# Optimization experiments

Hardware: AMD Instinct MI355X
Metric: run time of the kernel (lower is better)

Reference implementation:

```python
import jax, jax.numpy as jnp
import numpy as np

B, T, N, D = 32, 336, 321, 3
G = 512          # global_hidden
L = 2            # layer_nums
E = 4            # experts per layer
K = 2            # top-k
F = 2048         # d_ff (expert hidden)
P = 96           # pred_len
LOSS_COEF = 0.01


def setup_inputs() -> dict:
    key = jax.random.key(0)
    ks = iter(jax.random.split(key, 24))
    rn = lambda shape, s=0.02: jax.random.normal(next(ks), shape, jnp.float32) * s
    return {
        "x": jax.random.normal(next(ks), (B, T, N, D), jnp.float32),
        # GlobalEmbedding
        "Wv": rn((N, 1)), "bv": jnp.zeros((1,), jnp.float32),
        "Wt": rn((T, G)), "bt": jnp.zeros((G,), jnp.float32),
        # CrossAttention
        "Wq": rn((G, G)), "bq": jnp.zeros((G,), jnp.float32),
        "Wk": rn((G, G)), "bk": jnp.zeros((G,), jnp.float32),
        "Wva": rn((G, G)), "bva": jnp.zeros((G,), jnp.float32),
        # AMS MoE layers (stacked over L)
        "Wg": rn((L, T, E)),
        "We1": rn((L, E, T, F)), "be1": jnp.zeros((L, E, F), jnp.float32),
        "We2": rn((L, E, F, T)), "be2": jnp.zeros((L, E, T), jnp.float32),
        # projections head
        "P1w": rn((T, P)), "P1b": jnp.zeros((P,), jnp.float32),
        "P2w": rn((P, 2 * P)), "P2b": jnp.zeros((2 * P,), jnp.float32),
    }


def _cv_squared(v):
    return v.var() / (v.mean() ** 2 + 1e-10)


def reference(x, Wv, bv, Wt, bt, Wq, bq, Wk, bk, Wva, bva,
              Wg, We1, be1, We2, be2, P1w, P1b, P2w, P2b):
    Bv, Tv, Nv, Dv = x.shape
    # ---- GlobalEmbedding: (B,T,N,D) -> (B,D,G), with the original's raw reshape
    g = jnp.einsum('btvd,vo->btdo', x, Wv)[..., 0] + bv[0]        # (B,T,D)
    g2 = g.reshape(Bv * Dv, Tv) @ Wt + bt                          # faithful contiguous reshape
    gf = g2.reshape(Bv, Dv, -1)                                    # (B,D,G)
    # ---- CrossAttention (no sqrt(d) scaling, per source)
    q = gf @ Wq + bq
    kk = gf @ Wk + bk
    v = gf @ Wva + bva
    attn = jax.nn.softmax(jnp.einsum('big,bjg->bij', q, kk), axis=-1)
    sst_attended = jnp.einsum('bij,bjg->big', attn, v)[:, 0, :]    # unused: use_attend=0
    del sst_attended
    # ---- slice value channel + RevIN norm over time
    x0 = x[..., 0]                                                 # (B,T,N)
    mu = x0.mean(axis=1, keepdims=True)
    sd = jnp.sqrt(x0.var(axis=1, keepdims=True) + 1e-5)
    out = (x0 - mu) / sd
    # ---- AMS layers: clean top-k gated MoE over per-node seq MLP experts
    balance_loss = jnp.float32(0.0)
    for l in range(L):
        logits = out.mean(axis=2) @ Wg[l]                          # (B,E)
        topv, topi = jax.lax.top_k(logits, K)
        gates = jnp.zeros_like(logits).at[
            jnp.arange(Bv)[:, None], topi].set(jax.nn.softmax(topv, axis=-1))
        importance = gates.sum(axis=0)
        balance_loss = balance_loss + _cv_squared(importance) * LOSS_COEF
        xt = out.transpose(0, 2, 1)                                # (B,N,T)
        h = jax.nn.relu(jnp.einsum('bnt,etf->ebnf', xt, We1[l])
                        + be1[l][:, None, None, :])                # (E,B,N,F)
        eo = jnp.einsum('ebnf,eft->ebnt', h, We2[l]) + be2[l][:, None, None, :]
        moe = jnp.einsum('be,ebnt->bnt', gates, eo).transpose(0, 2, 1)
        out = out + moe                                            # residual_connection=1
    # ---- projection head
    o = out.transpose(0, 2, 1)                                     # (B,N,T)
    hproj = jnp.tanh(o @ P1w + P1b)
    p = (hproj @ P2w + P2b).reshape(Bv, Nv, P, 2).transpose(0, 2, 1, 3)  # (B,P,N,2)
    mean = p[..., 0]
    std = jax.nn.softplus(p[..., 1]) + 1e-6
    return mean, balance_loss, std
```

## Files before the change

kernel.cpp:

```cpp
#include <hip/hip_runtime.h>
#include <hip/hip_bf16.h>
#include <cstdint>
#include <math.h>

#define B_ 32
#define T_ 336
#define N_ 321
#define L_ 2
#define E_ 4
#define F_ 2048
#define P_ 96
#define TPAD 352
#define NPAD 384

typedef __hip_bfloat16 bf16;
typedef __attribute__((ext_vector_type(8))) __bf16 bf16x8;
typedef __attribute__((ext_vector_type(4))) float f32x4;


__device__ __forceinline__ void async_copy16(const void* g, void* l) {
  __builtin_amdgcn_global_load_lds(
      (__attribute__((address_space(1))) void*)(uintptr_t)g,
      (__attribute__((address_space(3))) void*)(unsigned int)(uintptr_t)l,
      16, 0, 0);
}

__device__ __forceinline__ void pipe_barrier_vm0() {
  asm volatile("s_waitcnt vmcnt(0)" ::: "memory");
  __builtin_amdgcn_s_barrier();
  __builtin_amdgcn_sched_barrier(0);
}

__device__ __forceinline__ void pipe_barrier_full() {
  asm volatile("s_waitcnt vmcnt(0) lgkmcnt(0)" ::: "memory");
  __builtin_amdgcn_s_barrier();
  __builtin_amdgcn_sched_barrier(0);
}

__global__ void transpose_cast_kernel(const float* __restrict__ src, bf16* __restrict__ dst,
                                      int R, int C, int Rp, int Cp,
                                      long long sStride, long long dStride) {
  __shared__ float tile[32][33];
  const float* s = src + (size_t)blockIdx.z * sStride;
  bf16* d = dst + (size_t)blockIdx.z * dStride;
  int r0 = blockIdx.x * 32, c0 = blockIdx.y * 32;
  int tx = threadIdx.x, ty = threadIdx.y;
  #pragma unroll
  for (int ii = 0; ii < 4; ii++) {
    int rl = ty * 4 + ii;
    int r = r0 + rl, c = c0 + tx;
    tile[rl][tx] = (r < R && c < C) ? s[(size_t)r * C + c] : 0.f;
  }
  __syncthreads();
  #pragma unroll
  for (int ii = 0; ii < 4; ii++) {
    int cl = ty * 4 + ii;
    int cd = c0 + cl, rd = r0 + tx;
    if (cd < Cp && rd < Rp)
      d[(size_t)cd * Rp + rd] = __float2bfloat16(tile[tx][cl]);
  }
}

__global__ void repack_w2_kernel(const float* __restrict__ src, bf16* __restrict__ dst) {
  __shared__ float tile[32][96];
  int le = blockIdx.z, tb = blockIdx.y, f0 = blockIdx.x * 32;
  int tid = threadIdx.x;
  const float* s = src + (size_t)le * F_ * T_;
  for (int idx = tid; idx < 32 * 96; idx += 256) {
    int ff = idx / 96, tt = idx % 96;
    int t = tb * 96 + tt;
    tile[ff][tt] = (t < T_) ? s[(size_t)(f0 + ff) * T_ + t] : 0.f;
  }
  __syncthreads();
  bf16* d = dst + ((size_t)le * 4 + tb) * 196608 + (size_t)(f0 >> 3) * 768;
  for (int s2 = tid; s2 < 384; s2 += 256) {
    int kgl = s2 / 96, row = s2 % 96;
    bf16 v[8];
    #pragma unroll
    for (int j = 0; j < 8; j++) v[j] = __float2bfloat16(tile[kgl * 8 + j][row]);
    *(uint4*)(d + (size_t)kgl * 768 + row * 8) = *(const uint4*)v;
  }
}

__global__ __launch_bounds__(512) void revin_kernel(const float* __restrict__ x,
                                                    float* __restrict__ out,
                                                    bf16* __restrict__ Abuf) {
  __shared__ float red[8][64][2];
  __shared__ float minv[64][2];
  __shared__ unsigned int Lt[64][177];

  const int b = blockIdx.x;
  const int n0 = blockIdx.y * 64;
  const int tid = threadIdx.x;
  const int nl = tid & 63, tq = tid >> 6;
  const int n = n0 + nl;
  const bool valid = (n < N_);
  const float* xp = x + ((size_t)b * T_ * N_ + n) * 3;
  const int tbeg = tq * 42, tend = tbeg + 42;

  float s1 = 0.f, s2 = 0.f;
  if (valid) {
    for (int t = tbeg; t < tend; t++) {
      float v = xp[(size_t)t * N_ * 3];
      s1 += v; s2 += v * v;
    }
  }
  red[tq][nl][0] = s1; red[tq][nl][1] = s2;
  __syncthreads();
  if (tid < 64) {
    float a = 0.f, c = 0.f;
    #pragma unroll
    for (int q = 0; q < 8; q++) { a += red[q][tid][0]; c += red[q][tid][1]; }
    float mu = a / (float)T_;
    float var = c / (float)T_ - mu * mu;
    minv[tid][0] = mu;
    minv[tid][1] = 1.f / sqrtf(var + 1e-5f);
  }
  {
    int r = tid >> 3, c = 168 + (tid & 7);
    Lt[r][c] = 0u;
  }
  __syncthreads();

  const float mu = minv[nl][0], inv = minv[nl][1];
  for (int t = tbeg; t < tend; t += 2) {
    float v0 = 0.f, v1 = 0.f;
    if (valid) {
      v0 = (xp[(size_t)t * N_ * 3] - mu) * inv;
      v1 = (xp[(size_t)(t + 1) * N_ * 3] - mu) * inv;
      out[((size_t)b * T_ + t) * N_ + n] = v0;
      out[((size_t)b * T_ + t + 1) * N_ + n] = v1;
    }
    bf16 h0 = __float2bfloat16(v0), h1 = __float2bfloat16(v1);
    unsigned int u = (unsigned int)*(unsigned short*)&h0 |
                     ((unsigned int)*(unsigned short*)&h1 << 16);
    Lt[nl][t >> 1] = u;
  }
  __syncthreads();

  unsigned int* abase = (unsigned int*)(Abuf + ((size_t)b * NPAD + n0) * TPAD);
  #pragma unroll
  for (int k = 0; k < 22; k++) {
    int idx = tid + k * 512;
    int row = idx / 176, c = idx % 176;
    abase[(size_t)row * (TPAD / 2) + c] = Lt[row][c];
  }
}

__global__ void gate1_kernel(const float* __restrict__ out, float* __restrict__ colsum) {
  int b = blockIdx.y;
  int w = threadIdx.x >> 6, lane = threadIdx.x & 63;
  int t = blockIdx.x * 16 + w * 4;
  #pragma unroll
  for (int i = 0; i < 4; i++, t++) {
    const float* p = out + ((size_t)b * T_ + t) * N_;
    float s = 0.f;
    for (int n = lane; n < N_; n += 64) s += p[n];
    #pragma unroll
    for (int off = 32; off; off >>= 1) s += __shfl_down(s, off);
    if (lane == 0) colsum[b * T_ + t] = s;
  }
}

__global__ void gate2_kernel(const float* __restrict__ colsum, const float* __restrict__ Wg,
                             int* __restrict__ pair_e, float* __restrict__ pair_gate,
                             float* __restrict__ loss_partial, int layer) {
  __shared__ float lg[32][4];
  __shared__ float gates[32][4];
  __shared__ float imp[4];
  int tid = threadIdx.x;
  if (tid < 128) {
    int b = tid >> 2, e = tid & 3;
    float s = 0.f;
    for (int t = 0; t < T_; t++)
      s += colsum[b * T_ + t] * Wg[(layer * T_ + t) * E_ + e];
    lg[b][e] = s / (float)N_;
  }
  __syncthreads();
  if (tid < 32) {
    float v[4];
    #pragma unroll
    for (int e = 0; e < 4; e++) v[e] = lg[tid][e];
    int i0 = 0;
    for (int e = 1; e < 4; e++) if (v[e] > v[i0]) i0 = e;
    int i1 = -1;
    for (int e = 0; e < 4; e++) {
      if (e == i0) continue;
      if (i1 < 0 || v[e] > v[i1]) i1 = e;
    }
    float ex = expf(v[i1] - v[i0]);
    float g0 = 1.f / (1.f + ex);
    float g1 = ex / (1.f + ex);
    pair_e[tid * 2] = i0; pair_e[tid * 2 + 1] = i1;
    pair_gate[tid * 2] = g0; pair_gate[tid * 2 + 1] = g1;
    #pragma unroll
    for (int e = 0; e < 4; e++) gates[tid][e] = 0.f;
    gates[tid][i0] = g0; gates[tid][i1] = g1;
  }
  __syncthreads();
  if (tid < 4) {
    float s = 0.f;
    for (int bb = 0; bb < 32; bb++) s += gates[bb][tid];
    imp[tid] = s;
  }
  __syncthreads();
  if (tid == 0) {
    float m = (imp[0] + imp[1] + imp[2] + imp[3]) * 0.25f;
    float va = 0.f;
    #pragma unroll
    for (int e = 0; e < 4; e++) { float d = imp[e] - m; va += d * d; }
    va *= 0.25f;
    loss_partial[layer] = 0.01f * (va / (m * m + 1e-10f));
  }
}

__global__ __launch_bounds__(256) void gemm1_kernel(
    const bf16* __restrict__ Abuf, const bf16* __restrict__ W1T,
    const float* __restrict__ be1, const int* __restrict__ pair_e,
    const float* __restrict__ pair_gate, bf16* __restrict__ h, int layer) {
  __shared__ __align__(16) bf16 S1[16384];
  __shared__ float bias_s[128];

  const int tid = threadIdx.x;
  const int w = tid >> 6, lane = tid & 63;
  const int pair = blockIdx.z;
  const int b = pair >> 1;
  const int e = pair_e[pair];
  const float gate = pair_gate[pair];
  const int m0 = blockIdx.y * 128;
  const int f0 = blockIdx.x * 128;

  const bf16* Ag = Abuf + (size_t)b * NPAD * TPAD + (size_t)m0 * TPAD;
  const bf16* Bg = W1T + ((size_t)(layer * E_ + e) * F_ + f0) * TPAD;
  if (tid < 128) bias_s[tid] = be1[(size_t)(layer * E_ + e) * F_ + f0 + tid];

  f32x4 acc[4][4];
  const f32x4 zero = {0.f, 0.f, 0.f, 0.f};
  #pragma unroll
  for (int i = 0; i < 4; i++)
    #pragma unroll
    for (int j = 0; j < 4; j++) acc[i][j] = zero;

  const int wm = w >> 1, wn = w & 1;
  const int lrow = lane >> 2;
  const int lkoff = (lane & 3) * 8;
  const int quad = lane >> 4;
  const int l15 = lane & 15;

  auto stage1 = [&](int k, int buf) {
    const int k0 = k * 32;
    bf16* As = S1 + buf * 8192;
    bf16* Bs = As + 4096;
    #pragma unroll
    for (int i = 0; i < 2; i++) {
      int r = (w * 2 + i) * 16 + lrow;
      async_copy16(Ag + (size_t)r * TPAD + k0 + lkoff, As + (w * 2 + i) * 512);
      async_copy16(Bg + (size_t)r * TPAD + k0 + lkoff, Bs + (w * 2 + i) * 512);
    }
  };

  stage1(0, 0);
  pipe_barrier_full();

  for (int kk = 0; kk < TPAD / 32; ++kk) {
    if (kk < TPAD / 32 - 1) stage1(kk + 1, (kk + 1) & 1);
    const bf16* As = S1 + (kk & 1) * 8192;
    const bf16* Bs = As + 4096;
    bf16x8 af[4], bfr[4];
    #pragma unroll
    for (int mi = 0; mi < 4; mi++)
      af[mi] = *(const bf16x8*)(As + (wm * 64 + mi * 16 + l15) * 32 + quad * 8);
    #pragma unroll
    for (int ni = 0; ni < 4; ni++)
      bfr[ni] = *(const bf16x8*)(Bs + (wn * 64 + ni * 16 + l15) * 32 + quad * 8);
    #pragma unroll
    for (int mi = 0; mi < 4; mi++)
      #pragma unroll
      for (int ni = 0; ni < 4; ni++)
        acc[mi][ni] = __builtin_amdgcn_mfma_f32_16x16x32_bf16(af[mi], bfr[ni], acc[mi][ni], 0, 0, 0);
    pipe_barrier_vm0();
  }

  bf16* tw0 = S1 + w * 1024;
  bf16* tw1 = S1 + 4096 + w * 1024;
  size_t hb = (size_t)pair * 786432 + (size_t)((m0 >> 6) + wm) * 131072;
  const int kgbase = (f0 >> 3) + wn * 8 + (lane & 3) * 2;
  #pragma unroll
  for (int mi = 0; mi < 4; mi++) {
    bf16* tw = (mi & 1) ? tw1 : tw0;
    #pragma unroll
    for (int ni = 0; ni < 4; ni++) {
      float bias = bias_s[wn * 64 + ni * 16 + l15];
      #pragma unroll
      for (int r = 0; r < 4; r++) {
        float v = acc[mi][ni][r] + bias;
        v = fmaxf(v, 0.f) * gate;
        tw[(quad * 4 + r) * 64 + ni * 16 + l15] = __float2bfloat16(v);
      }
    }
    int row = lane >> 2;
    int fpart = (lane & 3) * 16;
    const uint4* sp = (const uint4*)(tw + row * 64 + fpart);
    uint4 d0 = sp[0];
    uint4 d1 = sp[1];
    bf16* dp = h + hb + (size_t)kgbase * 512 + (mi * 16 + row) * 8;
    *(uint4*)dp = d0;
    *(uint4*)(dp + 512) = d1;
  }
}

#define CT_STRIDE 104
__global__ __launch_bounds__(256) void gemm2_kernel(
    const bf16* __restrict__ h, const bf16* __restrict__ W2B,
    const float* __restrict__ be2, const int* __restrict__ pair_e,
    const float* __restrict__ pair_gate, float* __restrict__ out,
    bf16* __restrict__ Abuf, int layer) {
  __shared__ __align__(16) bf16 S[20480];
  __shared__ float bias_t[96];

  const int tid = threadIdx.x;
  const int w = tid >> 6, lane = tid & 63;
  const int id = blockIdx.x;
  const int u = id & 7;
  const int v = id >> 3;
  const int tt = v & 3;
  const int pn = u + 8 * (v >> 2);
  const int b = pn / 6, nt = pn % 6;
  const int n0 = nt * 64, t0 = tt * 96;

  const int e0 = pair_e[b * 2], e1 = pair_e[b * 2 + 1];
  const float g0 = pair_gate[b * 2], g1 = pair_gate[b * 2 + 1];
  const bf16* Agb0 = h + ((size_t)(b * 2) * 6 + nt) * 131072;
  const bf16* Agb1 = h + ((size_t)(b * 2 + 1) * 6 + nt) * 131072;
  const bf16* Bgb0 = W2B + ((size_t)(layer * E_ + e0) * 4 + tt) * 196608;
  const bf16* Bgb1 = W2B + ((size_t)(layer * E_ + e1) * 4 + tt) * 196608;
  const int quad = lane >> 4, l15 = lane & 15;
  const int wm = w >> 1, wt = w & 1;

  if (tid < 96) {
    int t = t0 + tid;
    bias_t[tid] = (t < T_)
        ? g0 * be2[(layer * E_ + e0) * T_ + t] + g1 * be2[(layer * E_ + e1) * T_ + t]
        : 0.f;
  }

  f32x4 acc[2][3];
  const f32x4 zero = {0.f, 0.f, 0.f, 0.f};
  #pragma unroll
  for (int i = 0; i < 2; i++)
    #pragma unroll
    for (int jj = 0; jj < 3; jj++) acc[i][jj] = zero;

  auto stage2 = [&](int k, int buf) {
    const bf16* Aj = ((k < 32) ? Agb0 : Agb1) + (size_t)(k & 31) * 4096;
    const bf16* Bj = ((k < 32) ? Bgb0 : Bgb1) + (size_t)(k & 31) * 6144;
    bf16* As2 = S + buf * 10240;
    bf16* Bs2 = As2 + 4096;
    #pragma unroll
    for (int i = 0; i < 2; i++)
      async_copy16(Aj + (w * 2 + i) * 512 + lane * 8, As2 + (w * 2 + i) * 512);
    #pragma unroll
    for (int i = 0; i < 3; i++)
      async_copy16(Bj + (w * 3 + i) * 512 + lane * 8, Bs2 + (w * 3 + i) * 512);
  };

  stage2(0, 0);
  pipe_barrier_full();

  for (int kk = 0; kk < 64; ++kk) {
    if (kk < 63) stage2(kk + 1, (kk + 1) & 1);
    const bf16* As2 = S + (kk & 1) * 10240;
    const bf16* Bs2 = As2 + 4096;
    #pragma unroll
    for (int w32 = 0; w32 < 2; w32++) {
      const int kg = w32 * 4 + quad;
      bf16x8 af[2], bfr[3];
      #pragma unroll
      for (int mi = 0; mi < 2; mi++)
        af[mi] = *(const bf16x8*)(As2 + kg * 512 + (wm * 32 + mi * 16 + l15) * 8);
      #pragma unroll
      for (int ni = 0; ni < 3; ni++)
        bfr[ni] = *(const bf16x8*)(Bs2 + kg * 768 + (wt * 48 + ni * 16 + l15) * 8);
      #pragma unroll
      for (int mi = 0; mi < 2; mi++)
        #pragma unroll
        for (int ni = 0; ni < 3; ni++)
          acc[mi][ni] = __builtin_amdgcn_mfma_f32_16x16x32_bf16(af[mi], bfr[ni], acc[mi][ni], 0, 0, 0);
    }
    pipe_barrier_vm0();
  }

  #pragma unroll
  for (int mi = 0; mi < 2; mi++) {
    #pragma unroll
    for (int ni = 0; ni < 3; ni++) {
      int nloc_b = wm * 32 + mi * 16 + quad * 4;
      int tloc = wt * 48 + ni * 16 + l15;
      int t = t0 + tloc;
      #pragma unroll
      for (int r = 0; r < 4; r++) {
        int nloc = nloc_b + r;
        int n = n0 + nloc;
        float vv = 0.f;
        if (n < N_ && t < T_) {
          size_t q = ((size_t)b * T_ + t) * N_ + n;
          vv = out[q] + acc[mi][ni][r] + bias_t[tloc];
          out[q] = vv;
        }
        S[nloc * CT_STRIDE + tloc] = __float2bfloat16(vv);
      }
    }
  }
  __syncthreads();
  #pragma unroll
  for (int it = 0; it < 3; ++it) {
    int idx = tid + it * 256;
    int row = idx / 12, seg = idx % 12;
    int t = t0 + seg * 8;
    if (t < TPAD)
      *(uint4*)(Abuf + ((size_t)b * NPAD + n0 + row) * TPAD + t) =
          *(const uint4*)(S + row * CT_STRIDE + seg * 8);
  }
}

#define HS_STRIDE 104
__global__ __launch_bounds__(256) void proj_kernel(
    const bf16* __restrict__ Abuf, const bf16* __restrict__ P1T, const float* __restrict__ P1b,
    const bf16* __restrict__ P2T, const float* __restrict__ P2b,
    const float* __restrict__ loss_partial, float* __restrict__ dout) {
  __shared__ __align__(16) bf16 Hs[128 * HS_STRIDE];
  const int tid = threadIdx.x;
  const int w = tid >> 6, lane = tid & 63;
  const int quad = lane >> 4, l15 = lane & 15;
  const int b = blockIdx.y;
  const int m0 = blockIdx.x * 128;

  f32x4 acc1[2][6];
  const f32x4 zero = {0.f, 0.f, 0.f, 0.f};
  #pragma unroll
  for (int i = 0; i < 2; i++)
    #pragma unroll
    for (int j = 0; j < 6; j++) acc1[i][j] = zero;

  const bf16* Arow = Abuf + ((size_t)b * NPAD + m0 + w * 32) * TPAD;
  for (int kk = 0; kk < TPAD / 32; ++kk) {
    bf16x8 af[2], bfr[6];
    #pragma unroll
    for (int mi = 0; mi < 2; mi++)
      af[mi] = *(const bf16x8*)(Arow + (size_t)(mi * 16 + l15) * TPAD + kk * 32 + quad * 8);
    #pragma unroll
    for (int ni = 0; ni < 6; ni++)
      bfr[ni] = *(const bf16x8*)(P1T + (size_t)(ni * 16 + l15) * TPAD + kk * 32 + quad * 8);
    #pragma unroll
    for (int mi = 0; mi < 2; mi++)
      #pragma unroll
      for (int ni = 0; ni < 6; ni++)
        acc1[mi][ni] = __builtin_amdgcn_mfma_f32_16x16x32_bf16(af[mi], bfr[ni], acc1[mi][ni], 0, 0, 0);
  }

  #pragma unroll
  for (int mi = 0; mi < 2; mi++) {
    #pragma unroll
    for (int ni = 0; ni < 6; ni++) {
      float bias = P1b[ni * 16 + l15];
      #pragma unroll
      for (int r = 0; r < 4; r++) {
        float x = acc1[mi][ni][r] + bias;
        float t = 1.f - 2.f / (__expf(2.f * x) + 1.f);
        Hs[(w * 32 + mi * 16 + quad * 4 + r) * HS_STRIDE + ni * 16 + l15] = __float2bfloat16(t);
      }
    }
  }
  __syncthreads();

  #pragma unroll
  for (int half = 0; half < 2; ++half) {
    f32x4 acc2[2][6];
    #pragma unroll
    for (int i = 0; i < 2; i++)
      #pragma unroll
      for (int j = 0; j < 6; j++) acc2[i][j] = zero;

    #pragma unroll
    for (int kk = 0; kk < 3; ++kk) {
      bf16x8 af[2], bfr[6];
      #pragma unroll
      for (int mi = 0; mi < 2; mi++)
        af[mi] = *(const bf16x8*)(Hs + (w * 32 + mi * 16 + l15) * HS_STRIDE + kk * 32 + quad * 8);
      #pragma unroll
      for (int ni = 0; ni < 6; ni++)
        bfr[ni] = *(const bf16x8*)(P2T + (size_t)((half * 6 + ni) * 16 + l15) * P_ + kk * 32 + quad * 8);
      #pragma unroll
      for (int mi = 0; mi < 2; mi++)
        #pragma unroll
        for (int ni = 0; ni < 6; ni++)
          acc2[mi][ni] = __builtin_amdgcn_mfma_f32_16x16x32_bf16(af[mi], bfr[ni], acc2[mi][ni], 0, 0, 0);
    }

    #pragma unroll
    for (int mi = 0; mi < 2; mi++) {
      #pragma unroll
      for (int ni = 0; ni < 6; ni++) {
        int jj = (half * 6 + ni) * 16 + l15;
        float bias = P2b[jj];
        int pout = jj >> 1;
        #pragma unroll
        for (int r = 0; r < 4; r++) {
          int n = m0 + w * 32 + mi * 16 + quad * 4 + r;
          if (n < N_) {
            float s = acc2[mi][ni][r] + bias;
            size_t o = ((size_t)b * P_ + pout) * N_ + n;
            if ((jj & 1) == 0) {
              dout[o] = s;
            } else {
              float sp = (s > 20.f) ? s : log1pf(__expf(s));
              dout[(size_t)B_ * P_ * N_ + 1 + o] = sp + 1e-6f;
            }
          }
        }
      }
    }
  }
  if (b == 0 && blockIdx.x == 0 && tid == 0)
    dout[(size_t)B_ * P_ * N_] = loss_partial[0] + loss_partial[1];
}

extern "C" void kernel_launch(void* const* d_in, const int* in_sizes, int n_in,
                              void* d_out, int out_size, void* d_ws, size_t ws_size,
                              hipStream_t stream) {
  const float* x   = (const float*)d_in[0];
  const float* Wg  = (const float*)d_in[11];
  const float* We1 = (const float*)d_in[12];
  const float* be1 = (const float*)d_in[13];
  const float* We2 = (const float*)d_in[14];
  const float* be2 = (const float*)d_in[15];
  const float* P1w = (const float*)d_in[16];
  const float* P1b = (const float*)d_in[17];
  const float* P2w = (const float*)d_in[18];
  const float* P2b = (const float*)d_in[19];

  char* ws = (char*)d_ws;
  size_t off = 0;
  auto alloc = [&](size_t bytes) -> void* {
    void* p = ws + off;
    off += (bytes + 255) & ~(size_t)255;
    return p;
  };
  float* out        = (float*)alloc((size_t)B_ * T_ * N_ * 4);
  bf16*  Abuf       = (bf16*) alloc((size_t)B_ * NPAD * TPAD * 2);
  bf16*  W1T        = (bf16*) alloc((size_t)L_ * E_ * F_ * TPAD * 2);
  bf16*  W2B        = (bf16*) alloc((size_t)L_ * E_ * 4 * 196608 * 2);
  bf16*  P1T        = (bf16*) alloc((size_t)P_ * TPAD * 2);
  bf16*  P2T        = (bf16*) alloc((size_t)2 * P_ * P_ * 2);
  bf16*  h          = (bf16*) alloc((size_t)B_ * 2 * 786432 * 2);
  float* colsum     = (float*)alloc((size_t)B_ * T_ * 4);
  int*   pair_e     = (int*)  alloc(B_ * 2 * 4);
  float* pair_gate  = (float*)alloc(B_ * 2 * 4);
  float* loss_part  = (float*)alloc(2 * 4);
  if (ws_size < off) return;

  dim3 tb(32, 8);
  transpose_cast_kernel<<<dim3(11, 64, 8), tb, 0, stream>>>(
      We1, W1T, T_, F_, TPAD, F_, (long long)T_ * F_, (long long)F_ * TPAD);
  repack_w2_kernel<<<dim3(64, 4, 8), 256, 0, stream>>>(We2, W2B);
  transpose_cast_kernel<<<dim3(11, 3, 1), tb, 0, stream>>>(
      P1w, P1T, T_, P_, TPAD, P_, 0, 0);
  transpose_cast_kernel<<<dim3(3, 6, 1), tb, 0, stream>>>(
      P2w, P2T, P_, 2 * P_, P_, 2 * P_, 0, 0);

  revin_kernel<<<dim3(B_, 6), 512, 0, stream>>>(x, out, Abuf);

  for (int l = 0; l < L_; ++l) {
    gate1_kernel<<<dim3(21, B_), 256, 0, stream>>>(out, colsum);
    gate2_kernel<<<1, 128, 0, stream>>>(colsum, Wg, pair_e, pair_gate, loss_part, l);
    gemm1_kernel<<<dim3(16, 3, 64), 256, 0, stream>>>(Abuf, W1T, be1, pair_e, pair_gate, h, l);
    gemm2_kernel<<<768, 256, 0, stream>>>(h, W2B, be2, pair_e, pair_gate, out, Abuf, l);
  }

  proj_kernel<<<dim3(3, B_), 256, 0, stream>>>(Abuf, P1T, P1b, P2T, P2b, loss_part,
                                               (float*)d_out);
}
```

Measured before the change: 541.8 us.

## Use 32x32x16 MFMA with split-K across waves and LDS reduction in gemm2

The second expert GEMM moves from 16x16x32 MFMAs, where each wave owned a 32x48 output tile, to 32x32x16 MFMAs. Each wave now computes the full 64x96 tile over its own slice of K. The four per-wave partial accumulators are then reduced through LDS in several staged rounds, and only waves 0 and 1 run the epilogue. The aim is to cut LDS fragment reads per MFMA and use the larger MFMA shape, at the cost of more accumulator registers (96 floats per thread), a reduction phase with extra barriers, and an idle half of the block during the epilogue. Launch bounds now request 3 blocks per SM and the shared buffer grows to hold the reduction scratch.

```diff
diff --git a/kernel.cpp b/kernel.cpp
--- a/kernel.cpp
+++ b/kernel.cpp
@@ -16,6 +16,7 @@
 typedef __hip_bfloat16 bf16;
 typedef __attribute__((ext_vector_type(8))) __bf16 bf16x8;
 typedef __attribute__((ext_vector_type(4))) float f32x4;
+typedef __attribute__((ext_vector_type(16))) float f32x16;
 
 
 __device__ __forceinline__ void async_copy16(const void* g, void* l) {
@@ -310,16 +311,17 @@
 }
 
 #define CT_STRIDE 104
-__global__ __launch_bounds__(256) void gemm2_kernel(
+__global__ __launch_bounds__(256, 3) void gemm2_kernel(
     const bf16* __restrict__ h, const bf16* __restrict__ W2B,
     const float* __restrict__ be2, const int* __restrict__ pair_e,
     const float* __restrict__ pair_gate, float* __restrict__ out,
     bf16* __restrict__ Abuf, int layer) {
-  __shared__ __align__(16) bf16 S[20480];
+  __shared__ __align__(16) bf16 S[24576];
   __shared__ float bias_t[96];
 
   const int tid = threadIdx.x;
   const int w = tid >> 6, lane = tid & 63;
+  const int l31 = lane & 31, hi = lane >> 5;
   const int id = blockIdx.x;
   const int u = id & 7;
   const int v = id >> 3;
@@ -334,8 +336,6 @@
   const bf16* Agb1 = h + ((size_t)(b * 2 + 1) * 6 + nt) * 131072;
   const bf16* Bgb0 = W2B + ((size_t)(layer * E_ + e0) * 4 + tt) * 196608;
   const bf16* Bgb1 = W2B + ((size_t)(layer * E_ + e1) * 4 + tt) * 196608;
-  const int quad = lane >> 4, l15 = lane & 15;
-  const int wm = w >> 1, wt = w & 1;
 
   if (tid < 96) {
     int t = t0 + tid;
@@ -344,12 +344,16 @@
         : 0.f;
   }
 
-  f32x4 acc[2][3];
-  const f32x4 zero = {0.f, 0.f, 0.f, 0.f};
+  f32x16 acc[2][3];
   #pragma unroll
   for (int i = 0; i < 2; i++)
     #pragma unroll
-    for (int jj = 0; jj < 3; jj++) acc[i][jj] = zero;
+    for (int j = 0; j < 3; j++)
+      #pragma unroll
+      for (int r = 0; r < 16; r++) acc[i][j][r] = 0.f;
+
+  const int aoffA = (2 * w + hi) * 512;
+  const int boffB = (2 * w + hi) * 768;
 
   auto stage2 = [&](int k, int buf) {
     const bf16* Aj = ((k < 32) ? Agb0 : Agb1) + (size_t)(k & 31) * 4096;
@@ -364,54 +368,90 @@
       async_copy16(Bj + (w * 3 + i) * 512 + lane * 8, Bs2 + (w * 3 + i) * 512);
   };
 
+  auto compute = [&](int buf) {
+    const bf16* As2 = S + buf * 10240;
+    const bf16* Bs2 = As2 + 4096;
+    bf16x8 af[2], bfr[3];
+    #pragma unroll
+    for (int mi = 0; mi < 2; mi++)
+      af[mi] = *(const bf16x8*)(As2 + aoffA + (mi * 32 + l31) * 8);
+    #pragma unroll
+    for (int ni = 0; ni < 3; ni++)
+      bfr[ni] = *(const bf16x8*)(Bs2 + boffB + (ni * 32 + l31) * 8);
+    #pragma unroll
+    for (int mi = 0; mi < 2; mi++)
+      #pragma unroll
+      for (int ni = 0; ni < 3; ni++)
+        acc[mi][ni] = __builtin_amdgcn_mfma_f32_32x32x16_bf16(af[mi], bfr[ni], acc[mi][ni], 0, 0, 0);
+  };
+
   stage2(0, 0);
   pipe_barrier_full();
 
   for (int kk = 0; kk < 64; ++kk) {
     if (kk < 63) stage2(kk + 1, (kk + 1) & 1);
-    const bf16* As2 = S + (kk & 1) * 10240;
-    const bf16* Bs2 = As2 + 4096;
-    #pragma unroll
-    for (int w32 = 0; w32 < 2; w32++) {
-      const int kg = w32 * 4 + quad;
-      bf16x8 af[2], bfr[3];
-      #pragma unroll
-      for (int mi = 0; mi < 2; mi++)
-        af[mi] = *(const bf16x8*)(As2 + kg * 512 + (wm * 32 + mi * 16 + l15) * 8);
-      #pragma unroll
-      for (int ni = 0; ni < 3; ni++)
-        bfr[ni] = *(const bf16x8*)(Bs2 + kg * 768 + (wt * 48 + ni * 16 + l15) * 8);
-      #pragma unroll
-      for (int mi = 0; mi < 2; mi++)
+    compute(kk & 1);
+    pipe_barrier_vm0();
+  }
+
+  float* R = (float*)S;
+  auto dump3 = [&](float* dst, const f32x16 (&a)[3]) {
+    #pragma unroll
+    for (int ni = 0; ni < 3; ni++)
+      #pragma unroll
+      for (int rq = 0; rq < 4; rq++) {
+        f32x4 t4;
         #pragma unroll
-        for (int ni = 0; ni < 3; ni++)
-          acc[mi][ni] = __builtin_amdgcn_mfma_f32_16x16x32_bf16(af[mi], bfr[ni], acc[mi][ni], 0, 0, 0);
-    }
-    pipe_barrier_vm0();
-  }
-
-  #pragma unroll
-  for (int mi = 0; mi < 2; mi++) {
+        for (int j = 0; j < 4; j++) t4[j] = a[ni][rq * 4 + j];
+        *(f32x4*)(dst + (ni * 4 + rq) * 256 + lane * 4) = t4;
+      }
+  };
+  auto add3 = [&](const float* src, f32x16 (&a)[3]) {
+    #pragma unroll
+    for (int ni = 0; ni < 3; ni++)
+      #pragma unroll
+      for (int rq = 0; rq < 4; rq++) {
+        f32x4 t4 = *(const f32x4*)(src + (ni * 4 + rq) * 256 + lane * 4);
+        #pragma unroll
+        for (int j = 0; j < 4; j++) a[ni][rq * 4 + j] += t4[j];
+      }
+  };
+
+  if (w == 2) { dump3(R, acc[0]); dump3(R + 3072, acc[1]); }
+  if (w == 3) { dump3(R + 6144, acc[0]); dump3(R + 9216, acc[1]); }
+  __syncthreads();
+  if (w == 0) { add3(R, acc[0]); add3(R + 3072, acc[1]); }
+  if (w == 1) { add3(R + 6144, acc[0]); add3(R + 9216, acc[1]); }
+  __syncthreads();
+  if (w == 0) dump3(R, acc[1]);
+  if (w == 1) dump3(R + 3072, acc[0]);
+  __syncthreads();
+  if (w == 0) add3(R + 3072, acc[0]);
+  if (w == 1) add3(R, acc[1]);
+  __syncthreads();
+
+  auto epi = [&](const f32x16 (&a)[3], int nbase) {
     #pragma unroll
     for (int ni = 0; ni < 3; ni++) {
-      int nloc_b = wm * 32 + mi * 16 + quad * 4;
-      int tloc = wt * 48 + ni * 16 + l15;
-      int t = t0 + tloc;
-      #pragma unroll
-      for (int r = 0; r < 4; r++) {
-        int nloc = nloc_b + r;
-        int n = n0 + nloc;
+      #pragma unroll
+      for (int r = 0; r < 16; r++) {
+        int nloc = nbase + (r & 3) + 8 * (r >> 2) + 4 * hi;
+        int tloc = ni * 32 + l31;
+        int n = n0 + nloc, t = t0 + tloc;
         float vv = 0.f;
         if (n < N_ && t < T_) {
           size_t q = ((size_t)b * T_ + t) * N_ + n;
-          vv = out[q] + acc[mi][ni][r] + bias_t[tloc];
+          vv = out[q] + a[ni][r] + bias_t[tloc];
           out[q] = vv;
         }
         S[nloc * CT_STRIDE + tloc] = __float2bfloat16(vv);
       }
     }
-  }
-  __syncthreads();
+  };
+  if (w == 0) epi(acc[0], 0);
+  else if (w == 1) epi(acc[1], 32);
+  __syncthreads();
+
   #pragma unroll
   for (int it = 0; it < 3; ++it) {
     int idx = tid + it * 256;
```

Measured after the change: 693.8 us. 28.1% more time.
